# Kernel tuning notes

Hardware: AMD Instinct MI355X
Metric: run time of the kernel (lower is better)

Reference implementation:

```python
import jax, jax.numpy as jnp
import numpy as np

B, T, D, H, L = 8, 512, 768, 12, 12
OBS, VOCAB, MAXT, BLK = 128, 6, 4096, 1023
S = 2 * T          # interleaved state/action token sequence
DH = D // H
DFF = 4 * D


def _ln(x, g, b):
    m = jnp.mean(x, -1, keepdims=True)
    v = jnp.mean((x - m) ** 2, -1, keepdims=True)
    return (x - m) * jax.lax.rsqrt(v + 1e-5) * g + b


def setup_inputs() -> dict:
    key = jax.random.key(0)
    ks = jax.random.split(key, 24)
    p = lambda k, shape: (jax.random.normal(k, shape, jnp.float32) * 0.02)
    return {
        'states': jax.random.normal(ks[0], (B, T, OBS), jnp.float32),
        'actions': jax.random.randint(ks[1], (B, T, 1), 0, VOCAB),
        'timesteps': jax.random.randint(ks[2], (B, 1, 1), 0, MAXT + 1),
        'W_s': p(ks[3], (OBS, D)), 'b_s': jnp.zeros((D,), jnp.float32),
        'A_emb': p(ks[4], (VOCAB, D)),
        'pos_emb': p(ks[5], (1, BLK + 1, D)),
        'gpos_emb': p(ks[6], (1, MAXT + 1, D)),
        'ln1_g': jnp.ones((L, D), jnp.float32), 'ln1_b': jnp.zeros((L, D), jnp.float32),
        'Wq': p(ks[7], (L, D, D)), 'bq': jnp.zeros((L, D), jnp.float32),
        'Wk': p(ks[8], (L, D, D)), 'bk': jnp.zeros((L, D), jnp.float32),
        'Wv': p(ks[9], (L, D, D)), 'bv': jnp.zeros((L, D), jnp.float32),
        'Wp': p(ks[10], (L, D, D)), 'bp': jnp.zeros((L, D), jnp.float32),
        'ln2_g': jnp.ones((L, D), jnp.float32), 'ln2_b': jnp.zeros((L, D), jnp.float32),
        'W1': p(ks[11], (L, D, DFF)), 'b1': jnp.zeros((L, DFF), jnp.float32),
        'W2': p(ks[12], (L, DFF, D)), 'b2': jnp.zeros((L, D), jnp.float32),
        'lnf_g': jnp.ones((D,), jnp.float32), 'lnf_b': jnp.zeros((D,), jnp.float32),
    }


def reference(states, actions, timesteps, W_s, b_s, A_emb, pos_emb, gpos_emb,
              ln1_g, ln1_b, Wq, bq, Wk, bk, Wv, bv, Wp, bp,
              ln2_g, ln2_b, W1, b1, W2, b2, lnf_g, lnf_b):
    # encoders
    se = jnp.tanh(states @ W_s + b_s)                       # [B,T,D]
    ae = jnp.tanh(A_emb[actions[..., 0]])                   # [B,T,D]
    # interleave: s0,a0,s1,a1,... -> [B,S,D]
    tok = jnp.stack([se, ae], axis=2).reshape(B, S, D)
    # global positional (one timestep gathered per batch) + local positional
    gpos = gpos_emb[0][timesteps[:, 0, 0]][:, None, :]      # [B,1,D]
    x = tok + gpos + pos_emb[:, :S, :]
    mask = jnp.tril(jnp.ones((S, S), dtype=bool))
    scale = 1.0 / np.sqrt(DH).astype(np.float32)
    for l in range(L):
        h = _ln(x, ln1_g[l], ln1_b[l])
        q = (h @ Wq[l] + bq[l]).reshape(B, S, H, DH)
        k = (h @ Wk[l] + bk[l]).reshape(B, S, H, DH)
        v = (h @ Wv[l] + bv[l]).reshape(B, S, H, DH)
        att = jnp.einsum('bqhd,bkhd->bhqk', q, k) * scale
        att = jnp.where(mask[None, None], att, -jnp.inf)
        att = jax.nn.softmax(att, axis=-1)
        y = jnp.einsum('bhqk,bkhd->bqhd', att, v).reshape(B, S, D)
        x = x + y @ Wp[l] + bp[l]
        h = _ln(x, ln2_g[l], ln2_b[l])
        x = x + jax.nn.gelu(h @ W1[l] + b1[l], approximate=False) @ W2[l] + b2[l]
    x = _ln(x, lnf_g, lnf_b)
    return x[:, ::2, :]                                     # state_output [B,T,D]
```

## Files before the change

kernel.cpp:

```cpp
#include <hip/hip_runtime.h>
#include <hip/hip_bf16.h>

#define B_   8
#define T_   512
#define S_   1024
#define D_   768
#define H_   12
#define DH_  64
#define L_   12
#define DFF_ 3072
#define M_   8192
#define QKVD 2304

typedef float f32x4 __attribute__((ext_vector_type(4)));
typedef short b16x8 __attribute__((ext_vector_type(8)));
typedef short s16x4 __attribute__((ext_vector_type(4)));

#define LDS_CAST(p) ((__attribute__((address_space(3))) void*)(unsigned)(unsigned long long)(p))
#define GBL_CAST(p) ((const __attribute__((address_space(1))) void*)(unsigned long long)(p))

__device__ inline short f2b(float f) {
  unsigned u = __builtin_bit_cast(unsigned, f);
  unsigned r = u + 0x7fffu + ((u >> 16) & 1u);
  return (short)(unsigned short)(r >> 16);
}
__device__ inline float b2f(short s) {
  unsigned u = ((unsigned)(unsigned short)s) << 16;
  return __builtin_bit_cast(float, u);
}
__device__ inline float gelu_f(float v) {
  const float e = __expf(v * (1.5957691216f + 0.0713548162f * v * v));
  return v * e / (e + 1.0f);
}
__device__ inline float tanh_f(float v) {
  const float e = __expf(2.0f * v);
  return 1.0f - 2.0f / (e + 1.0f);
}

__global__ __launch_bounds__(256) void cvt_kernel(const float* __restrict__ in,
                                                  short* __restrict__ out, int n) {
  const int i = (blockIdx.x * 256 + threadIdx.x) * 4;
  if (i < n) {
    const f32x4 v = *(const f32x4*)&in[i];
    out[i] = f2b(v.x); out[i + 1] = f2b(v.y); out[i + 2] = f2b(v.z); out[i + 3] = f2b(v.w);
  }
}

__global__ __launch_bounds__(256) void trconv_kernel(const float* __restrict__ W,
                                                     short* __restrict__ Wt,
                                                     int K, int N) {
  __shared__ float tile[32][33];
  const int k0 = blockIdx.x * 32, n0 = blockIdx.y * 32;
  const int tx = threadIdx.x & 31, ty = threadIdx.x >> 5;
  #pragma unroll
  for (int i = ty; i < 32; i += 8) tile[i][tx] = W[(size_t)(k0 + i) * N + (n0 + tx)];
  __syncthreads();
  #pragma unroll
  for (int i = ty; i < 32; i += 8) Wt[(size_t)(n0 + i) * K + (k0 + tx)] = f2b(tile[tx][i]);
}

__global__ __launch_bounds__(256) void trconv_layer(const float* __restrict__ Wq,
                                                    const float* __restrict__ Wk,
                                                    const float* __restrict__ Wv,
                                                    const float* __restrict__ Wp,
                                                    const float* __restrict__ W1,
                                                    const float* __restrict__ W2,
                                                    short* __restrict__ Dqkv,
                                                    short* __restrict__ Dp,
                                                    short* __restrict__ D1,
                                                    short* __restrict__ D2) {
  __shared__ float tile[64][33];
  int id = blockIdx.x;
  const float* W; short* Dst; int K, N, kt, nt;
  if (id < 1152) {
    const int wsel = id / 288; id -= wsel * 288;
    W   = (wsel == 0) ? Wq : (wsel == 1) ? Wk : (wsel == 2) ? Wv : Wp;
    Dst = (wsel == 3) ? Dp : (Dqkv + (size_t)wsel * D_ * D_);
    K = D_; N = D_; kt = id / 24; nt = id % 24;
  } else if (id < 2304) {
    id -= 1152; W = W1; Dst = D1; K = D_; N = DFF_; kt = id / 96; nt = id % 96;
  } else {
    id -= 2304; W = W2; Dst = D2; K = DFF_; N = D_; kt = id / 24; nt = id % 24;
  }
  const int k0 = kt * 64, n0 = nt * 32;
  const int tid = threadIdx.x;
  const int tx = tid & 31, ty = tid >> 5;
  #pragma unroll
  for (int i = ty; i < 64; i += 8) tile[i][tx] = W[(size_t)(k0 + i) * N + (n0 + tx)];
  __syncthreads();
  const int iq = tid >> 4, q = tid & 15;
  #pragma unroll
  for (int s = 0; s < 2; ++s) {
    const int n = iq + 16 * s;
    s16x4 o4;
    o4.x = f2b(tile[q * 4 + 0][n]);
    o4.y = f2b(tile[q * 4 + 1][n]);
    o4.z = f2b(tile[q * 4 + 2][n]);
    o4.w = f2b(tile[q * 4 + 3][n]);
    *(s16x4*)&Dst[(size_t)(n0 + n) * K + k0 + q * 4] = o4;
  }
}

__global__ __launch_bounds__(256) void embed2_kernel(
    const short* __restrict__ se, const int* __restrict__ actions,
    const int* __restrict__ timesteps, const float* __restrict__ A_emb,
    const float* __restrict__ pos_emb, const float* __restrict__ gpos_emb,
    float* __restrict__ x) {
  const int bt = blockIdx.x;
  const int b = bt >> 9, t = bt & 511;
  const int tid = threadIdx.x;
  const int act = actions[bt];
  const int ts = timesteps[b];
  const float* gp = gpos_emb + (size_t)ts * D_;
  #pragma unroll
  for (int i = 0; i < 3; ++i) {
    const int d = tid + i * 256;
    const float sev = b2f(se[(size_t)bt * D_ + d]);
    const float aev = tanhf(A_emb[act * D_ + d]);
    const float g = gp[d];
    const size_t base = ((size_t)b * S_ + 2 * t) * D_ + d;
    x[base]      = sev + g + pos_emb[(2 * t) * D_ + d];
    x[base + D_] = aev + g + pos_emb[(2 * t + 1) * D_ + d];
  }
}

__global__ __launch_bounds__(256) void ln_kernel(const float* __restrict__ x,
                                                 const float* __restrict__ gg,
                                                 const float* __restrict__ bb,
                                                 short* __restrict__ out) {
  __shared__ float red[4];
  const int row = blockIdx.x, tid = threadIdx.x;
  const float* xr = x + (size_t)row * D_;
  f32x4 v = {0.f, 0.f, 0.f, 0.f};
  if (tid < 192) v = *(const f32x4*)&xr[tid * 4];
  float s = v.x + v.y + v.z + v.w;
  #pragma unroll
  for (int o = 32; o > 0; o >>= 1) s += __shfl_xor(s, o);
  if ((tid & 63) == 0) red[tid >> 6] = s;
  __syncthreads();
  const float mean = (red[0] + red[1] + red[2] + red[3]) * (1.0f / D_);
  __syncthreads();
  const f32x4 d = {v.x - mean, v.y - mean, v.z - mean, v.w - mean};
  float s2 = (tid < 192) ? (d.x * d.x + d.y * d.y + d.z * d.z + d.w * d.w) : 0.f;
  #pragma unroll
  for (int o = 32; o > 0; o >>= 1) s2 += __shfl_xor(s2, o);
  if ((tid & 63) == 0) red[tid >> 6] = s2;
  __syncthreads();
  const float inv = rsqrtf((red[0] + red[1] + red[2] + red[3]) * (1.0f / D_) + 1e-5f);
  if (tid < 192) {
    const f32x4 g = *(const f32x4*)&gg[tid * 4];
    const f32x4 b = *(const f32x4*)&bb[tid * 4];
    s16x4 o4;
    o4.x = f2b(d.x * inv * g.x + b.x);
    o4.y = f2b(d.y * inv * g.y + b.y);
    o4.z = f2b(d.z * inv * g.z + b.z);
    o4.w = f2b(d.w * inv * g.w + b.w);
    *(s16x4*)&out[(size_t)row * D_ + tid * 4] = o4;
  }
}

template <int MODE>
__global__ __launch_bounds__(256) void reduce2_kernel(
    const float* __restrict__ P, const float* __restrict__ bias,
    float* __restrict__ x, const float* __restrict__ gg,
    const float* __restrict__ bb, short* __restrict__ h,
    float* __restrict__ out) {
  __shared__ float red[4];
  const int row = (MODE == 2) ? (blockIdx.x * 2) : blockIdx.x;
  const int tid = threadIdx.x;
  const float* p0 = P + (size_t)row * D_;
  const float* p1 = P + (size_t)M_ * D_ + (size_t)row * D_;
  float* xr = x + (size_t)row * D_;
  f32x4 v = {0.f, 0.f, 0.f, 0.f};
  if (tid < 192) {
    const f32x4 a = *(const f32x4*)&xr[tid * 4];
    const f32x4 q0 = *(const f32x4*)&p0[tid * 4];
    const f32x4 q1 = *(const f32x4*)&p1[tid * 4];
    const f32x4 bv = *(const f32x4*)&bias[tid * 4];
    v.x = a.x + q0.x + q1.x + bv.x;
    v.y = a.y + q0.y + q1.y + bv.y;
    v.z = a.z + q0.z + q1.z + bv.z;
    v.w = a.w + q0.w + q1.w + bv.w;
    if (MODE == 1) *(f32x4*)&xr[tid * 4] = v;
  }
  float s = v.x + v.y + v.z + v.w;
  #pragma unroll
  for (int o = 32; o > 0; o >>= 1) s += __shfl_xor(s, o);
  if ((tid & 63) == 0) red[tid >> 6] = s;
  __syncthreads();
  const float mean = (red[0] + red[1] + red[2] + red[3]) * (1.0f / D_);
  __syncthreads();
  const f32x4 d = {v.x - mean, v.y - mean, v.z - mean, v.w - mean};
  float s2 = (tid < 192) ? (d.x * d.x + d.y * d.y + d.z * d.z + d.w * d.w) : 0.f;
  #pragma unroll
  for (int o = 32; o > 0; o >>= 1) s2 += __shfl_xor(s2, o);
  if ((tid & 63) == 0) red[tid >> 6] = s2;
  __syncthreads();
  const float inv = rsqrtf((red[0] + red[1] + red[2] + red[3]) * (1.0f / D_) + 1e-5f);
  if (tid < 192) {
    const f32x4 g = *(const f32x4*)&gg[tid * 4];
    const f32x4 b = *(const f32x4*)&bb[tid * 4];
    if (MODE == 1) {
      s16x4 o4;
      o4.x = f2b(d.x * inv * g.x + b.x);
      o4.y = f2b(d.y * inv * g.y + b.y);
      o4.z = f2b(d.z * inv * g.z + b.z);
      o4.w = f2b(d.w * inv * g.w + b.w);
      *(s16x4*)&h[(size_t)row * D_ + tid * 4] = o4;
    } else {
      const int bb2 = row >> 10, t = (row & 1023) >> 1;
      f32x4 o4;
      o4.x = d.x * inv * g.x + b.x;
      o4.y = d.y * inv * g.y + b.y;
      o4.z = d.z * inv * g.z + b.z;
      o4.w = d.w * inv * g.w + b.w;
      *(f32x4*)&out[((size_t)bb2 * T_ + t) * D_ + tid * 4] = o4;
    }
  }
}

__device__ __forceinline__ void mainloop128(const short* __restrict__ gA,
                                            const short* __restrict__ gB,
                                            int K, int kIters,
                                            short* As, short* Bs,
                                            int wave, int l15, int lq, int wr, int wc,
                                            f32x4 (&acc)[4][4]) {
  auto STAGE = [&](int kt, int buf) {
    const short* a = gA + kt * 32;
    const short* b = gB + kt * 32;
    short* la = As + buf * 4096 + wave * 512;
    short* lb = Bs + buf * 4096 + wave * 512;
    __builtin_amdgcn_global_load_lds(GBL_CAST(a),                  LDS_CAST(la),        16, 0, 0);
    __builtin_amdgcn_global_load_lds(GBL_CAST(a + (size_t)64 * K), LDS_CAST(la + 2048), 16, 0, 0);
    __builtin_amdgcn_global_load_lds(GBL_CAST(b),                  LDS_CAST(lb),        16, 0, 0);
    __builtin_amdgcn_global_load_lds(GBL_CAST(b + (size_t)64 * K), LDS_CAST(lb + 2048), 16, 0, 0);
  };
  STAGE(0, 0);
  __syncthreads();
  int cur = 0;
  for (int kt = 0; kt < kIters; ++kt) {
    if (kt + 1 < kIters) STAGE(kt + 1, cur ^ 1);
    const short* Ab = As + cur * 4096;
    const short* Bb = Bs + cur * 4096;
    b16x8 af[4], bfr[4];
    #pragma unroll
    for (int i = 0; i < 4; ++i)
      af[i] = *(const b16x8*)&Ab[(wr * 64 + i * 16 + l15) * 32 + lq * 8];
    #pragma unroll
    for (int j = 0; j < 4; ++j)
      bfr[j] = *(const b16x8*)&Bb[(wc * 64 + j * 16 + l15) * 32 + lq * 8];
    __builtin_amdgcn_s_setprio(1);
    #pragma unroll
    for (int i = 0; i < 4; ++i)
      #pragma unroll
      for (int j = 0; j < 4; ++j)
        acc[i][j] = __builtin_amdgcn_mfma_f32_16x16x32_bf16(af[i], bfr[j], acc[i][j], 0, 0, 0);
    __builtin_amdgcn_s_setprio(0);
    __syncthreads();
    cur ^= 1;
  }
}

template <int EPI>
__global__ __launch_bounds__(256) void gemm_bf16(const short* __restrict__ A,
                                                 const short* __restrict__ Bt,
                                                 const float* __restrict__ bias,
                                                 short* __restrict__ Cb,
                                                 int M, int N, int K) {
  __shared__ __align__(16) short As[8192];
  __shared__ __align__(16) short Bs[8192];
  const int tid = threadIdx.x;
  const int wave = tid >> 6, lane = tid & 63;
  const int l15 = lane & 15, lq = lane >> 4;
  const int wr = wave >> 1, wc = wave & 1;
  const int row0 = blockIdx.x * 128, col0 = blockIdx.y * 128;

  const short* gA = A + (size_t)(row0 + (tid >> 2)) * K + (tid & 3) * 8;
  const short* gB = Bt + (size_t)(col0 + (tid >> 2)) * K + (tid & 3) * 8;
  f32x4 acc[4][4] = {};
  mainloop128(gA, gB, K, K / 32, As, Bs, wave, l15, lq, wr, wc, acc);

  #pragma unroll
  for (int i = 0; i < 4; ++i) {
    #pragma unroll
    for (int j = 0; j < 4; ++j) {
      const int col = col0 + wc * 64 + j * 16 + l15;
      const float bv = bias[col];
      #pragma unroll
      for (int r = 0; r < 4; ++r) {
        const int row = row0 + wr * 64 + i * 16 + lq * 4 + r;
        const float v = acc[i][j][r] + bv;
        const size_t idx = (size_t)row * N + col;
        if (EPI == 1) Cb[idx] = f2b(gelu_f(v));
        else          Cb[idx] = f2b(tanh_f(v));
      }
    }
  }
}

__global__ __launch_bounds__(256) void gemm_splitk(const short* __restrict__ A,
                                                   const short* __restrict__ Bt,
                                                   float* __restrict__ P,
                                                   int M, int N, int K, int KC) {
  __shared__ __align__(16) short As[8192];
  __shared__ __align__(16) short Bs[8192];
  const int tid = threadIdx.x;
  const int wave = tid >> 6, lane = tid & 63;
  const int l15 = lane & 15, lq = lane >> 4;
  const int wr = wave >> 1, wc = wave & 1;
  const int row0 = blockIdx.x * 128, col0 = blockIdx.y * 128;
  const int k0 = blockIdx.z * KC;

  const short* gA = A + (size_t)(row0 + (tid >> 2)) * K + (tid & 3) * 8 + k0;
  const short* gB = Bt + (size_t)(col0 + (tid >> 2)) * K + (tid & 3) * 8 + k0;
  f32x4 acc[4][4] = {};
  mainloop128(gA, gB, K, KC / 32, As, Bs, wave, l15, lq, wr, wc, acc);

  float* Pz = P + (size_t)blockIdx.z * M * N;
  #pragma unroll
  for (int i = 0; i < 4; ++i) {
    #pragma unroll
    for (int j = 0; j < 4; ++j) {
      const int col = col0 + wc * 64 + j * 16 + l15;
      #pragma unroll
      for (int r = 0; r < 4; ++r) {
        const int row = row0 + wr * 64 + i * 16 + lq * 4 + r;
        Pz[(size_t)row * N + col] = acc[i][j][r];
      }
    }
  }
}

__global__ __launch_bounds__(256) void gemm_qkv(const short* __restrict__ A,
                                                const short* __restrict__ Bt,
                                                const float* __restrict__ bq,
                                                const float* __restrict__ bk,
                                                const float* __restrict__ bv,
                                                short* __restrict__ Cb, int K) {
  __shared__ __align__(16) short As[8192];
  __shared__ __align__(16) short Bs[8192];
  const int tid = threadIdx.x;
  const int wave = tid >> 6, lane = tid & 63;
  const int l15 = lane & 15, lq = lane >> 4;
  const int wr = wave >> 1, wc = wave & 1;
  const int row0 = blockIdx.x * 128, col0 = blockIdx.y * 128;
  const int seg = col0 / D_;
  const float* bias = (seg == 0) ? bq : (seg == 1) ? bk : bv;
  const float scale = (seg == 0) ? 0.125f : 1.0f;

  const short* gA = A + (size_t)(row0 + (tid >> 2)) * K + (tid & 3) * 8;
  const short* gB = Bt + (size_t)(col0 + (tid >> 2)) * K + (tid & 3) * 8;
  f32x4 acc[4][4] = {};
  mainloop128(gA, gB, K, K / 32, As, Bs, wave, l15, lq, wr, wc, acc);

  #pragma unroll
  for (int i = 0; i < 4; ++i) {
    #pragma unroll
    for (int j = 0; j < 4; ++j) {
      const int col = col0 + wc * 64 + j * 16 + l15;
      const float bv = bias[col - seg * D_];
      #pragma unroll
      for (int r = 0; r < 4; ++r) {
        const int row = row0 + wr * 64 + i * 16 + lq * 4 + r;
        Cb[(size_t)row * QKVD + col] = f2b((acc[i][j][r] + bv) * scale);
      }
    }
  }
}

__global__ __launch_bounds__(256) void gemm64(const short* __restrict__ A,
                                              const short* __restrict__ Bt,
                                              const float* __restrict__ bias,
                                              float* __restrict__ Xres,
                                              int M, int N, int K) {
  __shared__ __align__(16) short As[4096];
  __shared__ __align__(16) short Bs[8192];
  const int tid = threadIdx.x;
  const int wave = tid >> 6, lane = tid & 63;
  const int l15 = lane & 15, lq = lane >> 4;
  const int wr = wave >> 1, wc = wave & 1;
  const int row0 = blockIdx.x * 64, col0 = blockIdx.y * 128;

  const short* gA = A + (size_t)(row0 + (tid >> 2)) * K + (tid & 3) * 8;
  const short* gB = Bt + (size_t)(col0 + (tid >> 2)) * K + (tid & 3) * 8;

  auto STAGE = [&](int kt, int buf) {
    const short* a = gA + kt * 32;
    const short* b = gB + kt * 32;
    short* la = As + buf * 2048 + wave * 512;
    short* lb = Bs + buf * 4096 + wave * 512;
    __builtin_amdgcn_global_load_lds(GBL_CAST(a),                  LDS_CAST(la),        16, 0, 0);
    __builtin_amdgcn_global_load_lds(GBL_CAST(b),                  LDS_CAST(lb),        16, 0, 0);
    __builtin_amdgcn_global_load_lds(GBL_CAST(b + (size_t)64 * K), LDS_CAST(lb + 2048), 16, 0, 0);
  };

  f32x4 acc[2][4] = {};
  STAGE(0, 0);
  __syncthreads();
  int cur = 0;
  const int kIters = K / 32;
  for (int kt = 0; kt < kIters; ++kt) {
    if (kt + 1 < kIters) STAGE(kt + 1, cur ^ 1);
    const short* Ab = As + cur * 2048;
    const short* Bb = Bs + cur * 4096;
    b16x8 af[2], bfr[4];
    #pragma unroll
    for (int i = 0; i < 2; ++i)
      af[i] = *(const b16x8*)&Ab[(wr * 32 + i * 16 + l15) * 32 + lq * 8];
    #pragma unroll
    for (int j = 0; j < 4; ++j)
      bfr[j] = *(const b16x8*)&Bb[(wc * 64 + j * 16 + l15) * 32 + lq * 8];
    __builtin_amdgcn_s_setprio(1);
    #pragma unroll
    for (int i = 0; i < 2; ++i)
      #pragma unroll
      for (int j = 0; j < 4; ++j)
        acc[i][j] = __builtin_amdgcn_mfma_f32_16x16x32_bf16(af[i], bfr[j], acc[i][j], 0, 0, 0);
    __builtin_amdgcn_s_setprio(0);
    __syncthreads();
    cur ^= 1;
  }
  #pragma unroll
  for (int i = 0; i < 2; ++i) {
    #pragma unroll
    for (int j = 0; j < 4; ++j) {
      const int col = col0 + wc * 64 + j * 16 + l15;
      const float bv = bias[col];
      #pragma unroll
      for (int r = 0; r < 4; ++r) {
        const int row = row0 + wr * 32 + i * 16 + lq * 4 + r;
        Xres[(size_t)row * N + col] += acc[i][j][r] + bv;
      }
    }
  }
}

__global__ __launch_bounds__(256) void attn_kernel(const short* __restrict__ qkv,
                                                   short* __restrict__ yb) {
  __shared__ __align__(16) short Ks[2][4096];
  __shared__ __align__(16) short Vt[2][64 * 72];
  __shared__ __align__(16) short Ps[4][16 * 88];

  const int bh = blockIdx.x, pair = blockIdx.y;
  const int h = bh % H_, b = bh / H_;
  const int tid = threadIdx.x, wave = tid >> 6, lane = tid & 63;
  const int l15 = lane & 15, lq = lane >> 4;

  const int r0 = tid >> 3, c0 = tid & 7;
  const int r1 = (tid + 256) >> 3;
  const int vkey = tid >> 2, vdhg = tid & 3;

  for (int t2 = 0; t2 < 2; ++t2) {
    const int qt = t2 ? (15 - pair) : pair;
    const int nkt = qt + 1;
    const int qrow0 = qt * 64 + wave * 16;

    const short* qp = qkv + (size_t)(b * S_ + qrow0 + l15) * QKVD + h * 64 + lq * 8;
    const b16x8 qf0 = *(const b16x8*)qp;
    const b16x8 qf1 = *(const b16x8*)(qp + 32);

    f32x4 o[4] = {};
    float lacc[4] = {0.f, 0.f, 0.f, 0.f};

    auto stage = [&](int kt, int s) {
      const int kbase = kt * 64;
      const short* gk0 = qkv + (size_t)(b * S_ + kbase + r0) * QKVD + D_ + h * 64 + ((c0 ^ (r0 & 7)) * 8);
      __builtin_amdgcn_global_load_lds(GBL_CAST(gk0), LDS_CAST(&Ks[s][wave * 512]), 16, 0, 0);
      const short* gk1 = qkv + (size_t)(b * S_ + kbase + r1) * QKVD + D_ + h * 64 + ((c0 ^ (r1 & 7)) * 8);
      __builtin_amdgcn_global_load_lds(GBL_CAST(gk1), LDS_CAST(&Ks[s][2048 + wave * 512]), 16, 0, 0);
      const short* gv = qkv + (size_t)(b * S_ + kbase + vkey) * QKVD + 2 * D_ + h * 64 + vdhg * 16;
      const b16x8 v0 = *(const b16x8*)gv;
      const b16x8 v1 = *(const b16x8*)(gv + 8);
      #pragma unroll
      for (int e = 0; e < 8; ++e) Vt[s][(vdhg * 16 + e) * 72 + vkey] = v0[e];
      #pragma unroll
      for (int e = 0; e < 8; ++e) Vt[s][(vdhg * 16 + 8 + e) * 72 + vkey] = v1[e];
    };

    stage(0, 0);
    __syncthreads();

    for (int kt = 0; kt < nkt; ++kt) {
      const int cur = kt & 1;
      if (kt + 1 < nkt) stage(kt + 1, cur ^ 1);
      const int kbase = kt * 64;
      const bool needmask = (kt == qt);

      f32x4 s4[4];
      #pragma unroll
      for (int j = 0; j < 4; ++j) {
        const int krow = j * 16 + l15;
        const b16x8 kf0 = *(const b16x8*)&Ks[cur][krow * 64 + ((lq ^ (krow & 7)) * 8)];
        const b16x8 kf1 = *(const b16x8*)&Ks[cur][krow * 64 + (((4 + lq) ^ (krow & 7)) * 8)];
        f32x4 z = {};
        z = __builtin_amdgcn_mfma_f32_16x16x32_bf16(qf0, kf0, z, 0, 0, 0);
        s4[j] = __builtin_amdgcn_mfma_f32_16x16x32_bf16(qf1, kf1, z, 0, 0, 0);
      }

      #pragma unroll
      for (int r = 0; r < 4; ++r) {
        const int q = qrow0 + lq * 4 + r;
        float psum = 0.f;
        #pragma unroll
        for (int j = 0; j < 4; ++j) {
          float pp = __expf(s4[j][r]);
          if (needmask && (kbase + j * 16 + l15 > q)) pp = 0.f;
          psum += pp;
          Ps[wave][(lq * 4 + r) * 88 + j * 16 + l15] = f2b(pp);
        }
        lacc[r] += psum;
      }

      #pragma unroll
      for (int c = 0; c < 2; ++c) {
        const b16x8 pf = *(const b16x8*)&Ps[wave][l15 * 88 + c * 32 + lq * 8];
        #pragma unroll
        for (int jn = 0; jn < 4; ++jn) {
          const b16x8 vf = *(const b16x8*)&Vt[cur][(jn * 16 + l15) * 72 + c * 32 + lq * 8];
          o[jn] = __builtin_amdgcn_mfma_f32_16x16x32_bf16(pf, vf, o[jn], 0, 0, 0);
        }
      }
      __syncthreads();
    }

    #pragma unroll
    for (int r = 0; r < 4; ++r) {
      #pragma unroll
      for (int ofs = 1; ofs < 16; ofs <<= 1) lacc[r] += __shfl_xor(lacc[r], ofs);
      lacc[r] = 1.0f / lacc[r];
    }

    #pragma unroll
    for (int jn = 0; jn < 4; ++jn) {
      #pragma unroll
      for (int r = 0; r < 4; ++r) {
        const int q = qrow0 + lq * 4 + r;
        const int dh = jn * 16 + l15;
        yb[(size_t)(b * S_ + q) * D_ + h * 64 + dh] = f2b(o[jn][r] * lacc[r]);
      }
    }
  }
}

extern "C" void kernel_launch(void* const* d_in, const int* in_sizes, int n_in,
                              void* d_out, int out_size, void* d_ws, size_t ws_size,
                              hipStream_t stream) {
  (void)in_sizes; (void)n_in; (void)out_size; (void)ws_size;
  const float* states    = (const float*)d_in[0];
  const int*   actions   = (const int*)d_in[1];
  const int*   timesteps = (const int*)d_in[2];
  const float* W_s       = (const float*)d_in[3];
  const float* b_s       = (const float*)d_in[4];
  const float* A_emb     = (const float*)d_in[5];
  const float* pos_emb   = (const float*)d_in[6];
  const float* gpos_emb  = (const float*)d_in[7];
  const float* ln1_g     = (const float*)d_in[8];
  const float* ln1_b     = (const float*)d_in[9];
  const float* Wq        = (const float*)d_in[10];
  const float* bq        = (const float*)d_in[11];
  const float* Wk        = (const float*)d_in[12];
  const float* bk        = (const float*)d_in[13];
  const float* Wv        = (const float*)d_in[14];
  const float* bv        = (const float*)d_in[15];
  const float* Wp        = (const float*)d_in[16];
  const float* bp        = (const float*)d_in[17];
  const float* ln2_g     = (const float*)d_in[18];
  const float* ln2_b     = (const float*)d_in[19];
  const float* W1        = (const float*)d_in[20];
  const float* b1        = (const float*)d_in[21];
  const float* W2        = (const float*)d_in[22];
  const float* b2        = (const float*)d_in[23];
  const float* lnf_g     = (const float*)d_in[24];
  const float* lnf_b     = (const float*)d_in[25];
  float* out = (float*)d_out;

  char* p = (char*)d_ws;
  float* x    = (float*)p; p += (size_t)M_ * D_ * 4;
  short* h    = (short*)p; p += (size_t)M_ * D_ * 2;
  short* qkv  = (short*)p; p += (size_t)M_ * QKVD * 2;
  short* y    = (short*)p; p += (size_t)M_ * D_ * 2;
  short* gbf  = (short*)p; p += (size_t)M_ * DFF_ * 2;
  short* wqkvt= (short*)p; p += (size_t)QKVD * D_ * 2;
  short* wpt  = (short*)p; p += (size_t)D_ * D_ * 2;
  short* w1t  = (short*)p; p += (size_t)D_ * DFF_ * 2;
  short* w2t  = (short*)p; p += (size_t)D_ * DFF_ * 2;
  float* Pbuf = (float*)qkv;
  short* sbf  = qkv;
  short* wst  = qkv + (size_t)4096 * 128;
  short* se   = gbf;

  cvt_kernel<<<(B_ * T_ * 128) / 1024, 256, 0, stream>>>(states, sbf, B_ * T_ * 128);
  trconv_kernel<<<dim3(4, 24), 256, 0, stream>>>(W_s, wst, 128, D_);
  gemm_bf16<4><<<dim3(32, 6), 256, 0, stream>>>(sbf, wst, b_s, se, 4096, D_, 128);
  embed2_kernel<<<B_ * T_, 256, 0, stream>>>(se, actions, timesteps, A_emb, pos_emb, gpos_emb, x);
  ln_kernel<<<M_, 256, 0, stream>>>(x, ln1_g, ln1_b, h);

  for (int l = 0; l < L_; ++l) {
    trconv_layer<<<3456, 256, 0, stream>>>(
        Wq + (size_t)l * D_ * D_, Wk + (size_t)l * D_ * D_,
        Wv + (size_t)l * D_ * D_, Wp + (size_t)l * D_ * D_,
        W1 + (size_t)l * D_ * DFF_, W2 + (size_t)l * D_ * DFF_,
        wqkvt, wpt, w1t, w2t);

    gemm_qkv<<<dim3(M_ / 128, QKVD / 128), 256, 0, stream>>>(h, wqkvt, bq + l * D_, bk + l * D_, bv + l * D_, qkv, D_);
    attn_kernel<<<dim3(B_ * H_, 8), 256, 0, stream>>>(qkv, y);
    gemm64<<<dim3(M_ / 64, D_ / 128), 256, 0, stream>>>(y, wpt, bp + l * D_, x, M_, D_, D_);
    ln_kernel<<<M_, 256, 0, stream>>>(x, ln2_g + l * D_, ln2_b + l * D_, h);
    gemm_bf16<1><<<dim3(M_ / 128, DFF_ / 128), 256, 0, stream>>>(h, w1t, b1 + l * DFF_, gbf, M_, DFF_, D_);
    gemm_splitk<<<dim3(M_ / 128, D_ / 128, 2), 256, 0, stream>>>(gbf, w2t, Pbuf, M_, D_, DFF_, DFF_ / 2);
    if (l < L_ - 1) {
      reduce2_kernel<1><<<M_, 256, 0, stream>>>(Pbuf, b2 + l * D_, x,
                                                ln1_g + (l + 1) * D_, ln1_b + (l + 1) * D_, h, nullptr);
    } else {
      reduce2_kernel<2><<<M_ / 2, 256, 0, stream>>>(Pbuf, b2 + l * D_, x, lnf_g, lnf_b, nullptr, out);
    }
  }
}
```

Baseline: 2.982 ms.

## Double GEMM K-tile to 64 and XOR-swizzle LDS layout

Measured after the change: 2.761 ms. -7.4%, faster.

```diff
diff --git a/kernel.cpp b/kernel.cpp
--- a/kernel.cpp
+++ b/kernel.cpp
@@ -226,36 +226,42 @@
                                             int wave, int l15, int lq, int wr, int wc,
                                             f32x4 (&acc)[4][4]) {
   auto STAGE = [&](int kt, int buf) {
-    const short* a = gA + kt * 32;
-    const short* b = gB + kt * 32;
-    short* la = As + buf * 4096 + wave * 512;
-    short* lb = Bs + buf * 4096 + wave * 512;
-    __builtin_amdgcn_global_load_lds(GBL_CAST(a),                  LDS_CAST(la),        16, 0, 0);
-    __builtin_amdgcn_global_load_lds(GBL_CAST(a + (size_t)64 * K), LDS_CAST(la + 2048), 16, 0, 0);
-    __builtin_amdgcn_global_load_lds(GBL_CAST(b),                  LDS_CAST(lb),        16, 0, 0);
-    __builtin_amdgcn_global_load_lds(GBL_CAST(b + (size_t)64 * K), LDS_CAST(lb + 2048), 16, 0, 0);
+    const short* a = gA + kt * 64;
+    const short* b = gB + kt * 64;
+    short* la = As + buf * 8192 + wave * 512;
+    short* lb = Bs + buf * 8192 + wave * 512;
+    #pragma unroll
+    for (int j = 0; j < 4; ++j) {
+      __builtin_amdgcn_global_load_lds(GBL_CAST(a + (size_t)(j * 32) * K), LDS_CAST(la + j * 2048), 16, 0, 0);
+      __builtin_amdgcn_global_load_lds(GBL_CAST(b + (size_t)(j * 32) * K), LDS_CAST(lb + j * 2048), 16, 0, 0);
+    }
   };
   STAGE(0, 0);
   __syncthreads();
   int cur = 0;
+  const int swz = l15 & 7;
   for (int kt = 0; kt < kIters; ++kt) {
     if (kt + 1 < kIters) STAGE(kt + 1, cur ^ 1);
-    const short* Ab = As + cur * 4096;
-    const short* Bb = Bs + cur * 4096;
-    b16x8 af[4], bfr[4];
-    #pragma unroll
-    for (int i = 0; i < 4; ++i)
-      af[i] = *(const b16x8*)&Ab[(wr * 64 + i * 16 + l15) * 32 + lq * 8];
-    #pragma unroll
-    for (int j = 0; j < 4; ++j)
-      bfr[j] = *(const b16x8*)&Bb[(wc * 64 + j * 16 + l15) * 32 + lq * 8];
-    __builtin_amdgcn_s_setprio(1);
-    #pragma unroll
-    for (int i = 0; i < 4; ++i)
+    const short* Ab = As + cur * 8192;
+    const short* Bb = Bs + cur * 8192;
+    #pragma unroll
+    for (int s = 0; s < 2; ++s) {
+      const int ck = ((s * 4 + lq) ^ swz) * 8;
+      b16x8 af[4], bfr[4];
+      #pragma unroll
+      for (int i = 0; i < 4; ++i)
+        af[i] = *(const b16x8*)&Ab[(wr * 64 + i * 16 + l15) * 64 + ck];
       #pragma unroll
       for (int j = 0; j < 4; ++j)
-        acc[i][j] = __builtin_amdgcn_mfma_f32_16x16x32_bf16(af[i], bfr[j], acc[i][j], 0, 0, 0);
-    __builtin_amdgcn_s_setprio(0);
+        bfr[j] = *(const b16x8*)&Bb[(wc * 64 + j * 16 + l15) * 64 + ck];
+      __builtin_amdgcn_s_setprio(1);
+      #pragma unroll
+      for (int i = 0; i < 4; ++i)
+        #pragma unroll
+        for (int j = 0; j < 4; ++j)
+          acc[i][j] = __builtin_amdgcn_mfma_f32_16x16x32_bf16(af[i], bfr[j], acc[i][j], 0, 0, 0);
+      __builtin_amdgcn_s_setprio(0);
+    }
     __syncthreads();
     cur ^= 1;
   }
@@ -267,18 +273,20 @@
                                                  const float* __restrict__ bias,
                                                  short* __restrict__ Cb,
                                                  int M, int N, int K) {
-  __shared__ __align__(16) short As[8192];
-  __shared__ __align__(16) short Bs[8192];
+  __shared__ __align__(16) short As[16384];
+  __shared__ __align__(16) short Bs[16384];
   const int tid = threadIdx.x;
   const int wave = tid >> 6, lane = tid & 63;
   const int l15 = lane & 15, lq = lane >> 4;
   const int wr = wave >> 1, wc = wave & 1;
   const int row0 = blockIdx.x * 128, col0 = blockIdx.y * 128;
-
-  const short* gA = A + (size_t)(row0 + (tid >> 2)) * K + (tid & 3) * 8;
-  const short* gB = Bt + (size_t)(col0 + (tid >> 2)) * K + (tid & 3) * 8;
+  const int srow = wave * 8 + (lane >> 3);
+  const int acs = ((lane & 7) ^ ((lane >> 3) & 7)) * 8;
+
+  const short* gA = A + (size_t)(row0 + srow) * K + acs;
+  const short* gB = Bt + (size_t)(col0 + srow) * K + acs;
   f32x4 acc[4][4] = {};
-  mainloop128(gA, gB, K, K / 32, As, Bs, wave, l15, lq, wr, wc, acc);
+  mainloop128(gA, gB, K, K / 64, As, Bs, wave, l15, lq, wr, wc, acc);
 
   #pragma unroll
   for (int i = 0; i < 4; ++i) {
@@ -302,19 +310,21 @@
                                                    const short* __restrict__ Bt,
                                                    float* __restrict__ P,
                                                    int M, int N, int K, int KC) {
-  __shared__ __align__(16) short As[8192];
-  __shared__ __align__(16) short Bs[8192];
+  __shared__ __align__(16) short As[16384];
+  __shared__ __align__(16) short Bs[16384];
   const int tid = threadIdx.x;
   const int wave = tid >> 6, lane = tid & 63;
   const int l15 = lane & 15, lq = lane >> 4;
   const int wr = wave >> 1, wc = wave & 1;
   const int row0 = blockIdx.x * 128, col0 = blockIdx.y * 128;
   const int k0 = blockIdx.z * KC;
-
-  const short* gA = A + (size_t)(row0 + (tid >> 2)) * K + (tid & 3) * 8 + k0;
-  const short* gB = Bt + (size_t)(col0 + (tid >> 2)) * K + (tid & 3) * 8 + k0;
+  const int srow = wave * 8 + (lane >> 3);
+  const int acs = ((lane & 7) ^ ((lane >> 3) & 7)) * 8;
+
+  const short* gA = A + (size_t)(row0 + srow) * K + acs + k0;
+  const short* gB = Bt + (size_t)(col0 + srow) * K + acs + k0;
   f32x4 acc[4][4] = {};
-  mainloop128(gA, gB, K, KC / 32, As, Bs, wave, l15, lq, wr, wc, acc);
+  mainloop128(gA, gB, K, KC / 64, As, Bs, wave, l15, lq, wr, wc, acc);
 
   float* Pz = P + (size_t)blockIdx.z * M * N;
   #pragma unroll
@@ -337,8 +347,8 @@
                                                 const float* __restrict__ bk,
                                                 const float* __restrict__ bv,
                                                 short* __restrict__ Cb, int K) {
-  __shared__ __align__(16) short As[8192];
-  __shared__ __align__(16) short Bs[8192];
+  __shared__ __align__(16) short As[16384];
+  __shared__ __align__(16) short Bs[16384];
   const int tid = threadIdx.x;
   const int wave = tid >> 6, lane = tid & 63;
   const int l15 = lane & 15, lq = lane >> 4;
@@ -347,11 +357,13 @@
   const int seg = col0 / D_;
   const float* bias = (seg == 0) ? bq : (seg == 1) ? bk : bv;
   const float scale = (seg == 0) ? 0.125f : 1.0f;
-
-  const short* gA = A + (size_t)(row0 + (tid >> 2)) * K + (tid & 3) * 8;
-  const short* gB = Bt + (size_t)(col0 + (tid >> 2)) * K + (tid & 3) * 8;
+  const int srow = wave * 8 + (lane >> 3);
+  const int acs = ((lane & 7) ^ ((lane >> 3) & 7)) * 8;
+
+  const short* gA = A + (size_t)(row0 + srow) * K + acs;
+  const short* gB = Bt + (size_t)(col0 + srow) * K + acs;
   f32x4 acc[4][4] = {};
-  mainloop128(gA, gB, K, K / 32, As, Bs, wave, l15, lq, wr, wc, acc);
+  mainloop128(gA, gB, K, K / 64, As, Bs, wave, l15, lq, wr, wc, acc);
 
   #pragma unroll
   for (int i = 0; i < 4; ++i) {
@@ -373,50 +385,60 @@
                                               const float* __restrict__ bias,
                                               float* __restrict__ Xres,
                                               int M, int N, int K) {
-  __shared__ __align__(16) short As[4096];
-  __shared__ __align__(16) short Bs[8192];
+  __shared__ __align__(16) short As[8192];
+  __shared__ __align__(16) short Bs[16384];
   const int tid = threadIdx.x;
   const int wave = tid >> 6, lane = tid & 63;
   const int l15 = lane & 15, lq = lane >> 4;
   const int wr = wave >> 1, wc = wave & 1;
   const int row0 = blockIdx.x * 64, col0 = blockIdx.y * 128;
-
-  const short* gA = A + (size_t)(row0 + (tid >> 2)) * K + (tid & 3) * 8;
-  const short* gB = Bt + (size_t)(col0 + (tid >> 2)) * K + (tid & 3) * 8;
+  const int srow = wave * 8 + (lane >> 3);
+  const int acs = ((lane & 7) ^ ((lane >> 3) & 7)) * 8;
+
+  const short* gA = A + (size_t)(row0 + srow) * K + acs;
+  const short* gB = Bt + (size_t)(col0 + srow) * K + acs;
 
   auto STAGE = [&](int kt, int buf) {
-    const short* a = gA + kt * 32;
-    const short* b = gB + kt * 32;
-    short* la = As + buf * 2048 + wave * 512;
-    short* lb = Bs + buf * 4096 + wave * 512;
-    __builtin_amdgcn_global_load_lds(GBL_CAST(a),                  LDS_CAST(la),        16, 0, 0);
-    __builtin_amdgcn_global_load_lds(GBL_CAST(b),                  LDS_CAST(lb),        16, 0, 0);
-    __builtin_amdgcn_global_load_lds(GBL_CAST(b + (size_t)64 * K), LDS_CAST(lb + 2048), 16, 0, 0);
+    const short* a = gA + kt * 64;
+    const short* b = gB + kt * 64;
+    short* la = As + buf * 4096 + wave * 512;
+    short* lb = Bs + buf * 8192 + wave * 512;
+    #pragma unroll
+    for (int j = 0; j < 2; ++j)
+      __builtin_amdgcn_global_load_lds(GBL_CAST(a + (size_t)(j * 32) * K), LDS_CAST(la + j * 2048), 16, 0, 0);
+    #pragma unroll
+    for (int j = 0; j < 4; ++j)
+      __builtin_amdgcn_global_load_lds(GBL_CAST(b + (size_t)(j * 32) * K), LDS_CAST(lb + j * 2048), 16, 0, 0);
   };
 
   f32x4 acc[2][4] = {};
   STAGE(0, 0);
   __syncthreads();
   int cur = 0;
-  const int kIters = K / 32;
+  const int kIters = K / 64;
+  const int swz = l15 & 7;
   for (int kt = 0; kt < kIters; ++kt) {
     if (kt + 1 < kIters) STAGE(kt + 1, cur ^ 1);
-    const short* Ab = As + cur * 2048;
-    const short* Bb = Bs + cur * 4096;
-    b16x8 af[2], bfr[4];
-    #pragma unroll
-    for (int i = 0; i < 2; ++i)
-      af[i] = *(const b16x8*)&Ab[(wr * 32 + i * 16 + l15) * 32 + lq * 8];
-    #pragma unroll
-    for (int j = 0; j < 4; ++j)
-      bfr[j] = *(const b16x8*)&Bb[(wc * 64 + j * 16 + l15) * 32 + lq * 8];
-    __builtin_amdgcn_s_setprio(1);
-    #pragma unroll
-    for (int i = 0; i < 2; ++i)
+    const short* Ab = As + cur * 4096;
+    const short* Bb = Bs + cur * 8192;
+    #pragma unroll
+    for (int s = 0; s < 2; ++s) {
+      const int ck = ((s * 4 + lq) ^ swz) * 8;
+      b16x8 af[2], bfr[4];
+      #pragma unroll
+      for (int i = 0; i < 2; ++i)
+        af[i] = *(const b16x8*)&Ab[(wr * 32 + i * 16 + l15) * 64 + ck];
       #pragma unroll
       for (int j = 0; j < 4; ++j)
-        acc[i][j] = __builtin_amdgcn_mfma_f32_16x16x32_bf16(af[i], bfr[j], acc[i][j], 0, 0, 0);
-    __builtin_amdgcn_s_setprio(0);
+        bfr[j] = *(const b16x8*)&Bb[(wc * 64 + j * 16 + l15) * 64 + ck];
+      __builtin_amdgcn_s_setprio(1);
+      #pragma unroll
+      for (int i = 0; i < 2; ++i)
+        #pragma unroll
+        for (int j = 0; j < 4; ++j)
+          acc[i][j] = __builtin_amdgcn_mfma_f32_16x16x32_bf16(af[i], bfr[j], acc[i][j], 0, 0, 0);
+      __builtin_amdgcn_s_setprio(0);
+    }
     __syncthreads();
     cur ^= 1;
   }
```
